# Performance work log

Measured on AMD Instinct MI355X. Metric: run time of the kernel, lower is better.

The kernel has to match this reference:

```python
import jax, jax.numpy as jnp
import numpy as np

H = 1024
NH = 16
HD = H // NH
EPS = 1e-5

def setup_inputs() -> dict:
    key = jax.random.key(0)
    ks = jax.random.split(key, 5)
    B, S = 2, 2048
    scale = 1.0 / np.sqrt(H)
    return {
        "x": jax.random.normal(ks[0], (B, S, H), dtype=jnp.float32),
        "Wq": jax.random.normal(ks[1], (H, H), dtype=jnp.float32) * scale,
        "Wk": jax.random.normal(ks[2], (H, H), dtype=jnp.float32) * scale,
        "Wv": jax.random.normal(ks[3], (H, H), dtype=jnp.float32) * scale,
        "Wo": jax.random.normal(ks[4], (H, H), dtype=jnp.float32) * scale,
        "bo": jnp.zeros((H,), dtype=jnp.float32),
        "gamma": jnp.ones((H,), dtype=jnp.float32),
        "beta": jnp.zeros((H,), dtype=jnp.float32),
    }

def reference(x, Wq, Wk, Wv, Wo, bo, gamma, beta):
    B, S, _ = x.shape
    residual = x
    # pre-LayerNorm
    mu = jnp.mean(x, axis=-1, keepdims=True)
    var = jnp.mean(jnp.square(x - mu), axis=-1, keepdims=True)
    xn = (x - mu) * jax.lax.rsqrt(var + EPS) * gamma + beta
    # QKV projections (torch Linear: y = x @ W.T), split heads -> [B, NH, S, HD]
    q = (xn @ Wq.T).reshape(B, S, NH, HD).transpose(0, 2, 1, 3)
    k = (xn @ Wk.T).reshape(B, S, NH, HD).transpose(0, 2, 1, 3)
    v = (xn @ Wv.T).reshape(B, S, NH, HD).transpose(0, 2, 1, 3)
    # naive attention: explicit [B, NH, S, S] scores
    scale = 1.0 / np.sqrt(HD)
    scores = jnp.einsum('bhqd,bhkd->bhqk', q, k) * scale
    attn = jax.nn.softmax(scores.astype(jnp.float32), axis=-1).astype(q.dtype)
    out = jnp.einsum('bhqk,bhkd->bhqd', attn, v)
    out = out.transpose(0, 2, 1, 3).reshape(B, S, H)
    out = out @ Wo.T + bo
    return out + residual
```

## Files before the change

kernel.cpp:

```cpp
#include <hip/hip_runtime.h>
#include <hip/hip_bf16.h>

#define H 1024
#define NHEAD 16
#define HDIM 64
#define SEQ 2048
#define BATCH 2
#define M_TOT (BATCH * SEQ)
#define NQKV 3072

typedef __attribute__((ext_vector_type(8))) short bf16x8;
typedef __attribute__((ext_vector_type(4))) float f32x4;
typedef __attribute__((ext_vector_type(16))) float f32x16;

#define C2_SCALE 0.18033688f

__device__ __forceinline__ unsigned short f2bf(float f) {
  union { float f; unsigned int u; } a;
  a.f = f;
  unsigned int u = a.u;
  return (unsigned short)((u + 0x7fffu + ((u >> 16) & 1u)) >> 16);
}

__device__ __forceinline__ unsigned int pkbf(float a, float b) {
  union { __hip_bfloat162 h; unsigned int u; } cv;
  cv.h = __float22bfloat162_rn(float2{a, b});
  return cv.u;
}

__device__ __forceinline__ float fast_exp2(float x) {
#if defined(__has_builtin) && __has_builtin(__builtin_amdgcn_exp2f)
  return __builtin_amdgcn_exp2f(x);
#else
  return exp2f(x);
#endif
}

typedef const __attribute__((address_space(1))) void* gas1_t;
typedef __attribute__((address_space(3))) void* las3_t;
__device__ __forceinline__ void gload16(const void* g, void* l) {
  __builtin_amdgcn_global_load_lds((gas1_t)(unsigned long long)g,
                                   (las3_t)(unsigned int)(unsigned long long)l,
                                   16, 0, 0);
}

__global__ __launch_bounds__(256) void ln_cast_kernel(const float* __restrict__ x,
                                                      const float* __restrict__ gamma,
                                                      const float* __restrict__ beta,
                                                      unsigned short* __restrict__ xn,
                                                      const float* __restrict__ w0,
                                                      const float* __restrict__ w1,
                                                      const float* __restrict__ w2,
                                                      const float* __restrict__ w3,
                                                      unsigned short* __restrict__ wdst) {
  const int t = threadIdx.x;
  if (blockIdx.x >= M_TOT) {
    const int cb = blockIdx.x - M_TOT;
    const int y = cb >> 10;
    const float* s = (y == 0) ? w0 : (y == 1) ? w1 : (y == 2) ? w2 : w3;
    const int i = (cb & 1023) * 256 + t;
    const float4 v = ((const float4*)s)[i];
    ushort4 o;
    o.x = f2bf(v.x);
    o.y = f2bf(v.y);
    o.z = f2bf(v.z);
    o.w = f2bf(v.w);
    ((ushort4*)(wdst + (size_t)y * H * H))[i] = o;
    return;
  }
  const int row = blockIdx.x;
  const float* xr = x + (size_t)row * H;
  float4 v = ((const float4*)xr)[t];
  float s = v.x + v.y + v.z + v.w;
  float s2 = v.x * v.x + v.y * v.y + v.z * v.z + v.w * v.w;
#pragma unroll
  for (int o = 32; o; o >>= 1) {
    s += __shfl_xor(s, o, 64);
    s2 += __shfl_xor(s2, o, 64);
  }
  __shared__ float red[8];
  const int wave = t >> 6;
  if ((t & 63) == 0) {
    red[wave] = s;
    red[wave + 4] = s2;
  }
  __syncthreads();
  const float ts = red[0] + red[1] + red[2] + red[3];
  const float ts2 = red[4] + red[5] + red[6] + red[7];
  const float mu = ts * (1.0f / (float)H);
  const float var = ts2 * (1.0f / (float)H) - mu * mu;
  const float rstd = rsqrtf(var + 1e-5f);
  const float4 g = ((const float4*)gamma)[t];
  const float4 b = ((const float4*)beta)[t];
  ushort4 o;
  o.x = f2bf((v.x - mu) * rstd * g.x + b.x);
  o.y = f2bf((v.y - mu) * rstd * g.y + b.y);
  o.z = f2bf((v.z - mu) * rstd * g.z + b.z);
  o.w = f2bf((v.w - mu) * rstd * g.w + b.w);
  ((ushort4*)(xn + (size_t)row * H))[t] = o;
}

template <int EPI, int NPX>
__global__ __launch_bounds__(256, 4) void gemm128(const unsigned short* __restrict__ A,
                                                  const unsigned short* __restrict__ W,
                                                  unsigned short* __restrict__ qk,
                                                  unsigned short* __restrict__ vt,
                                                  const float* __restrict__ bo,
                                                  const float* __restrict__ x,
                                                  float* __restrict__ out) {
  const int id = blockIdx.x;
  const int xcd = id & 7;
  const int r = id >> 3;
  const int nb = xcd * NPX + (r % NPX);
  const int mb = r / NPX;
  const int m0 = mb * 128;
  const int n0 = nb * 128;
  const int tid = threadIdx.x;
  const int wave = tid >> 6;
  const int lane = tid & 63;
  const int l16 = lane & 15;
  const int quad = lane >> 4;
  const int wx = wave & 1, wy = wave >> 1;

  __shared__ __align__(16) unsigned short As[2][128 * 32];
  __shared__ __align__(16) unsigned short Bs[2][128 * 32];

  const int sub = lane >> 2;
  const int kcol = (lane & 3) * 8;
  const unsigned short* ag = A + (size_t)(m0 + wave * 32 + sub) * H + kcol;
  const unsigned short* bg = W + (size_t)(n0 + wave * 32 + sub) * H + kcol;
  const int lofs = wave * 32 * 32;

  f32x4 acc[4][4] = {};

  gload16(ag, &As[0][lofs]);
  gload16(ag + 16 * H, &As[0][lofs + 16 * 32]);
  gload16(bg, &Bs[0][lofs]);
  gload16(bg + 16 * H, &Bs[0][lofs + 16 * 32]);

  for (int it = 0; it < H / 32; it++) {
    const int bi = it & 1;
    __syncthreads();
    if (it + 1 < H / 32) {
      const int k1 = (it + 1) * 32;
      gload16(ag + k1, &As[bi ^ 1][lofs]);
      gload16(ag + k1 + 16 * H, &As[bi ^ 1][lofs + 16 * 32]);
      gload16(bg + k1, &Bs[bi ^ 1][lofs]);
      gload16(bg + k1 + 16 * H, &Bs[bi ^ 1][lofs + 16 * 32]);
    }
    bf16x8 af[4], bf[4];
#pragma unroll
    for (int t = 0; t < 4; t++) {
      af[t] = *(const bf16x8*)&As[bi][(wy * 64 + t * 16 + l16) * 32 + quad * 8];
      bf[t] = *(const bf16x8*)&Bs[bi][(wx * 64 + t * 16 + l16) * 32 + quad * 8];
    }
#pragma unroll
    for (int i = 0; i < 4; i++)
#pragma unroll
      for (int j = 0; j < 4; j++)
        acc[i][j] = __builtin_amdgcn_mfma_f32_16x16x32_bf16(af[i], bf[j], acc[i][j], 0, 0, 0);
  }

  if (EPI == 0) {
#pragma unroll
    for (int j = 0; j < 4; j++) {
      const int cb = n0 + wx * 64 + j * 16;
      if (cb < 2048) {
        const float qs = (cb < 1024) ? C2_SCALE : 1.0f;
#pragma unroll
        for (int i = 0; i < 4; i++) {
          const int row = m0 + wy * 64 + i * 16 + quad * 4;
#pragma unroll
          for (int r2 = 0; r2 < 4; r2++)
            qk[(size_t)(row + r2) * 2048 + cb + l16] = f2bf(acc[i][j][r2] * qs);
        }
      } else {
        const int n = cb + l16 - 2048;
#pragma unroll
        for (int i = 0; i < 4; i++) {
          const int row0 = m0 + wy * 64 + i * 16 + quad * 4;
          const int b = row0 >> 11;
          const int s = row0 & 2047;
          ushort4 p;
          p.x = f2bf(acc[i][j][0]);
          p.y = f2bf(acc[i][j][1]);
          p.z = f2bf(acc[i][j][2]);
          p.w = f2bf(acc[i][j][3]);
          *(ushort4*)&vt[((size_t)b * 1024 + n) * SEQ + s] = p;
        }
      }
    }
  } else {
#pragma unroll
    for (int j = 0; j < 4; j++) {
      const int col = n0 + wx * 64 + j * 16 + l16;
      const float bv = bo[col];
#pragma unroll
      for (int i = 0; i < 4; i++) {
        const int row = m0 + wy * 64 + i * 16 + quad * 4;
#pragma unroll
        for (int r2 = 0; r2 < 4; r2++) {
          const size_t idx = (size_t)(row + r2) * H + col;
          out[idx] = acc[i][j][r2] + bv + x[idx];
        }
      }
    }
  }
}

__global__ __launch_bounds__(256, 2) void attn_kernel(const unsigned short* __restrict__ qk,
                                                      const unsigned short* __restrict__ vt,
                                                      unsigned short* __restrict__ O) {
  const int id = blockIdx.x;
  const int xcd = id & 7;
  const int slot = id >> 3;
  const int qt = slot & 15;
  const int g = slot >> 4;
  const int combo = xcd * 4 + g;
  const int h = combo & 15;
  const int b = combo >> 4;
  const int tid = threadIdx.x;
  const int wave = tid >> 6;
  const int lane = tid & 63;
  const int l31 = lane & 31;
  const int l7 = lane & 7;
  const int hi = lane >> 5;

  __shared__ __align__(16) unsigned short Kt[2][64 * 64];
  __shared__ __align__(16) unsigned short Vt[2][64 * 64];

  const unsigned short* Qbase = qk + (size_t)b * SEQ * 2048 + h * 64;
  const unsigned short* Kbase = qk + (size_t)b * SEQ * 2048 + 1024 + h * 64;
  const unsigned short* Vbase = vt + ((size_t)b * 1024 + h * 64) * SEQ;

  const int rIn = lane >> 3;
  const int gsw = (lane & 7) ^ rIn;
  const int ch0 = 2 * wave;

  const int qrow = qt * 128 + wave * 32 + l31;
  bf16x8 aq[4];
#pragma unroll
  for (int kc = 0; kc < 4; kc++)
    aq[kc] = *(const bf16x8*)(Qbase + (size_t)qrow * 2048 + kc * 16 + hi * 8);

  f32x16 o_acc[2] = {};
  float lc[4] = {};

#pragma unroll
  for (int c = 0; c < 2; c++) {
    const int ch = ch0 + c;
    const int row = ch * 8 + rIn;
    gload16(Kbase + (size_t)row * 2048 + gsw * 8, &Kt[0][ch * 512]);
    gload16(Vbase + (size_t)row * SEQ + gsw * 8, &Vt[0][ch * 512]);
  }

#pragma unroll 2
  for (int it = 0; it < SEQ / 64; it++) {
    const int bi = it & 1;
    __syncthreads();
    if (it + 1 < SEQ / 64) {
#pragma unroll
      for (int c = 0; c < 2; c++) {
        const int ch = ch0 + c;
        const int row = ch * 8 + rIn;
        gload16(Kbase + (size_t)((it + 1) * 64 + row) * 2048 + gsw * 8,
                &Kt[bi ^ 1][ch * 512]);
        gload16(Vbase + (size_t)row * SEQ + (it + 1) * 64 + gsw * 8,
                &Vt[bi ^ 1][ch * 512]);
      }
    }

    f32x16 s_acc[2] = {};
#pragma unroll
    for (int kc = 0; kc < 4; kc++) {
#pragma unroll
      for (int mt = 0; mt < 2; mt++) {
        const bf16x8 kf = *(const bf16x8*)&Kt[bi][(mt * 32 + l31) * 64 +
                                                 ((kc * 16 + hi * 8) ^ (l7 * 8))];
        s_acc[mt] = __builtin_amdgcn_mfma_f32_32x32x16_bf16(kf, aq[kc], s_acc[mt], 0, 0, 0);
      }
    }

    unsigned int w[2][8];
#pragma unroll
    for (int mt = 0; mt < 2; mt++) {
      float p[16];
#pragma unroll
      for (int r2 = 0; r2 < 16; r2++) p[r2] = fast_exp2(s_acc[mt][r2]);
      const float a0 = (p[0] + p[1]) + (p[2] + p[3]);
      const float a1 = (p[4] + p[5]) + (p[6] + p[7]);
      const float a2 = (p[8] + p[9]) + (p[10] + p[11]);
      const float a3 = (p[12] + p[13]) + (p[14] + p[15]);
      lc[mt * 2 + 0] += a0 + a2;
      lc[mt * 2 + 1] += a1 + a3;
#pragma unroll
      for (int gi = 0; gi < 8; gi++) w[mt][gi] = pkbf(p[2 * gi], p[2 * gi + 1]);
    }

#pragma unroll
    for (int sc = 0; sc < 4; sc++) {
      const int n0i = 2 * sc, n1i = 2 * sc + 1;
      const int mt0 = n0i >> 2, b0 = n0i & 3;
      const int mt1 = n1i >> 2, b1 = n1i & 3;
      const auto rA = __builtin_amdgcn_permlane32_swap(w[mt0][2 * b0], w[mt1][2 * b1],
                                                       false, false);
      const auto rB = __builtin_amdgcn_permlane32_swap(w[mt0][2 * b0 + 1], w[mt1][2 * b1 + 1],
                                                       false, false);
      union { unsigned int u[4]; bf16x8 v; } pb;
      pb.u[0] = rA[0];
      pb.u[1] = rB[0];
      pb.u[2] = rA[1];
      pb.u[3] = rB[1];
#pragma unroll
      for (int dt = 0; dt < 2; dt++) {
        const bf16x8 vf = *(const bf16x8*)&Vt[bi][(dt * 32 + l31) * 64 +
                                                  ((sc * 16 + hi * 8) ^ (l7 * 8))];
        o_acc[dt] = __builtin_amdgcn_mfma_f32_32x32x16_bf16(vf, pb.v, o_acc[dt], 0, 0, 0);
      }
    }
  }

  float lsum = (lc[0] + lc[1]) + (lc[2] + lc[3]);
  const float l_i = lsum + __shfl_xor(lsum, 32, 64);
  const float inv = 1.0f / l_i;
  unsigned short* orow = O + ((size_t)(b * SEQ + qrow)) * H + h * 64;
#pragma unroll
  for (int dt = 0; dt < 2; dt++)
#pragma unroll
    for (int rg = 0; rg < 4; rg++) {
      uint2 d;
      d.x = pkbf(o_acc[dt][4 * rg + 0] * inv, o_acc[dt][4 * rg + 1] * inv);
      d.y = pkbf(o_acc[dt][4 * rg + 2] * inv, o_acc[dt][4 * rg + 3] * inv);
      *(uint2*)&orow[dt * 32 + 8 * rg + 4 * hi] = d;
    }
}

extern "C" void kernel_launch(void* const* d_in, const int* in_sizes, int n_in,
                              void* d_out, int out_size, void* d_ws, size_t ws_size,
                              hipStream_t stream) {
  const float* x = (const float*)d_in[0];
  const float* Wq = (const float*)d_in[1];
  const float* Wk = (const float*)d_in[2];
  const float* Wv = (const float*)d_in[3];
  const float* Wo = (const float*)d_in[4];
  const float* bo = (const float*)d_in[5];
  const float* gamma = (const float*)d_in[6];
  const float* beta = (const float*)d_in[7];
  float* out = (float*)d_out;

  unsigned short* ws = (unsigned short*)d_ws;
  unsigned short* xn = ws;
  unsigned short* wcat = xn + (size_t)M_TOT * H;
  unsigned short* wob = wcat + (size_t)3 * H * H;
  unsigned short* qkb = wcat + (size_t)4 * H * H;
  unsigned short* vtb = qkb + (size_t)M_TOT * 2048;
  unsigned short* atb = vtb + (size_t)BATCH * H * SEQ;

  ln_cast_kernel<<<M_TOT + 4096, 256, 0, stream>>>(x, gamma, beta, xn, Wq, Wk, Wv, Wo,
                                                   wcat);
  gemm128<0, 3><<<(M_TOT / 128) * (NQKV / 128), 256, 0, stream>>>(
      xn, wcat, qkb, vtb, nullptr, nullptr, nullptr);
  attn_kernel<<<(SEQ / 128) * NHEAD * BATCH, 256, 0, stream>>>(qkb, vtb, atb);
  gemm128<1, 1><<<(M_TOT / 128) * (H / 128), 256, 0, stream>>>(
      atb, wob, nullptr, nullptr, bo, x, out);
}
```

Before: 191.3 us.

## Split attention key tiles across wave pairs and shrink query tile to 64

The attention kernel now handles 64 query rows per block instead of 128. Each pair of waves splits every 64-key tile in half, so each wave computes one 32x32 score block instead of two. Partial O accumulators and row sums from waves 2-3 are reduced through shared memory, reusing the K buffer, before the normalized write. Grid size doubles and launch bounds go up to 4 blocks per CU to improve occupancy and parallelism, at the cost of loading each K/V tile twice as often per query row and adding a final reduction step.

```diff
diff --git a/kernel.cpp b/kernel.cpp
--- a/kernel.cpp
+++ b/kernel.cpp
@@ -208,14 +208,14 @@
   }
 }
 
-__global__ __launch_bounds__(256, 2) void attn_kernel(const unsigned short* __restrict__ qk,
+__global__ __launch_bounds__(256, 4) void attn_kernel(const unsigned short* __restrict__ qk,
                                                       const unsigned short* __restrict__ vt,
                                                       unsigned short* __restrict__ O) {
   const int id = blockIdx.x;
   const int xcd = id & 7;
   const int slot = id >> 3;
-  const int qt = slot & 15;
-  const int g = slot >> 4;
+  const int qt = slot & 31;
+  const int g = slot >> 5;
   const int combo = xcd * 4 + g;
   const int h = combo & 15;
   const int b = combo >> 4;
@@ -225,9 +225,12 @@
   const int l31 = lane & 31;
   const int l7 = lane & 7;
   const int hi = lane >> 5;
+  const int strip = wave & 1;
+  const int sh = wave >> 1;
 
   __shared__ __align__(16) unsigned short Kt[2][64 * 64];
   __shared__ __align__(16) unsigned short Vt[2][64 * 64];
+  __shared__ float lred[128];
 
   const unsigned short* Qbase = qk + (size_t)b * SEQ * 2048 + h * 64;
   const unsigned short* Kbase = qk + (size_t)b * SEQ * 2048 + 1024 + h * 64;
@@ -237,14 +240,14 @@
   const int gsw = (lane & 7) ^ rIn;
   const int ch0 = 2 * wave;
 
-  const int qrow = qt * 128 + wave * 32 + l31;
+  const int qrow = qt * 64 + strip * 32 + l31;
   bf16x8 aq[4];
 #pragma unroll
   for (int kc = 0; kc < 4; kc++)
     aq[kc] = *(const bf16x8*)(Qbase + (size_t)qrow * 2048 + kc * 16 + hi * 8);
 
   f32x16 o_acc[2] = {};
-  float lc[4] = {};
+  float lc[2] = {};
 
 #pragma unroll
   for (int c = 0; c < 2; c++) {
@@ -270,47 +273,41 @@
       }
     }
 
-    f32x16 s_acc[2] = {};
+    f32x16 s_acc = {};
 #pragma unroll
     for (int kc = 0; kc < 4; kc++) {
-#pragma unroll
-      for (int mt = 0; mt < 2; mt++) {
-        const bf16x8 kf = *(const bf16x8*)&Kt[bi][(mt * 32 + l31) * 64 +
-                                                 ((kc * 16 + hi * 8) ^ (l7 * 8))];
-        s_acc[mt] = __builtin_amdgcn_mfma_f32_32x32x16_bf16(kf, aq[kc], s_acc[mt], 0, 0, 0);
-      }
-    }
-
-    unsigned int w[2][8];
-#pragma unroll
-    for (int mt = 0; mt < 2; mt++) {
-      float p[16];
-#pragma unroll
-      for (int r2 = 0; r2 < 16; r2++) p[r2] = fast_exp2(s_acc[mt][r2]);
+      const bf16x8 kf = *(const bf16x8*)&Kt[bi][(sh * 32 + l31) * 64 +
+                                               ((kc * 16 + hi * 8) ^ (l7 * 8))];
+      s_acc = __builtin_amdgcn_mfma_f32_32x32x16_bf16(kf, aq[kc], s_acc, 0, 0, 0);
+    }
+
+    float p[16];
+#pragma unroll
+    for (int r2 = 0; r2 < 16; r2++) p[r2] = fast_exp2(s_acc[r2]);
+    {
       const float a0 = (p[0] + p[1]) + (p[2] + p[3]);
       const float a1 = (p[4] + p[5]) + (p[6] + p[7]);
       const float a2 = (p[8] + p[9]) + (p[10] + p[11]);
       const float a3 = (p[12] + p[13]) + (p[14] + p[15]);
-      lc[mt * 2 + 0] += a0 + a2;
-      lc[mt * 2 + 1] += a1 + a3;
-#pragma unroll
-      for (int gi = 0; gi < 8; gi++) w[mt][gi] = pkbf(p[2 * gi], p[2 * gi + 1]);
-    }
-
-#pragma unroll
-    for (int sc = 0; sc < 4; sc++) {
-      const int n0i = 2 * sc, n1i = 2 * sc + 1;
-      const int mt0 = n0i >> 2, b0 = n0i & 3;
-      const int mt1 = n1i >> 2, b1 = n1i & 3;
-      const auto rA = __builtin_amdgcn_permlane32_swap(w[mt0][2 * b0], w[mt1][2 * b1],
+      lc[0] += a0 + a2;
+      lc[1] += a1 + a3;
+    }
+    unsigned int w[8];
+#pragma unroll
+    for (int gi = 0; gi < 8; gi++) w[gi] = pkbf(p[2 * gi], p[2 * gi + 1]);
+
+#pragma unroll
+    for (int scp = 0; scp < 2; scp++) {
+      const auto rA = __builtin_amdgcn_permlane32_swap(w[4 * scp + 0], w[4 * scp + 2],
                                                        false, false);
-      const auto rB = __builtin_amdgcn_permlane32_swap(w[mt0][2 * b0 + 1], w[mt1][2 * b1 + 1],
+      const auto rB = __builtin_amdgcn_permlane32_swap(w[4 * scp + 1], w[4 * scp + 3],
                                                        false, false);
       union { unsigned int u[4]; bf16x8 v; } pb;
       pb.u[0] = rA[0];
       pb.u[1] = rB[0];
       pb.u[2] = rA[1];
       pb.u[3] = rB[1];
+      const int sc = sh * 2 + scp;
 #pragma unroll
       for (int dt = 0; dt < 2; dt++) {
         const bf16x8 vf = *(const bf16x8*)&Vt[bi][(dt * 32 + l31) * 64 +
@@ -320,19 +317,46 @@
     }
   }
 
-  float lsum = (lc[0] + lc[1]) + (lc[2] + lc[3]);
-  const float l_i = lsum + __shfl_xor(lsum, 32, 64);
-  const float inv = 1.0f / l_i;
-  unsigned short* orow = O + ((size_t)(b * SEQ + qrow)) * H + h * 64;
-#pragma unroll
-  for (int dt = 0; dt < 2; dt++)
-#pragma unroll
-    for (int rg = 0; rg < 4; rg++) {
-      uint2 d;
-      d.x = pkbf(o_acc[dt][4 * rg + 0] * inv, o_acc[dt][4 * rg + 1] * inv);
-      d.y = pkbf(o_acc[dt][4 * rg + 2] * inv, o_acc[dt][4 * rg + 3] * inv);
-      *(uint2*)&orow[dt * 32 + 8 * rg + 4 * hi] = d;
-    }
+  float lsum = lc[0] + lc[1];
+  __syncthreads();
+  if (wave >= 2) {
+    float4* obuf4 = (float4*)&Kt[0][0] + (size_t)(wave - 2) * 512;
+#pragma unroll
+    for (int dt = 0; dt < 2; dt++)
+#pragma unroll
+      for (int rg = 0; rg < 4; rg++)
+        obuf4[(dt * 4 + rg) * 64 + lane] =
+            float4{o_acc[dt][4 * rg + 0], o_acc[dt][4 * rg + 1],
+                   o_acc[dt][4 * rg + 2], o_acc[dt][4 * rg + 3]};
+    lred[(wave - 2) * 64 + lane] = lsum;
+  }
+  __syncthreads();
+  if (wave < 2) {
+    const float4* obuf4 = (const float4*)&Kt[0][0] + (size_t)wave * 512;
+#pragma unroll
+    for (int dt = 0; dt < 2; dt++)
+#pragma unroll
+      for (int rg = 0; rg < 4; rg++) {
+        const float4 pv4 = obuf4[(dt * 4 + rg) * 64 + lane];
+        o_acc[dt][4 * rg + 0] += pv4.x;
+        o_acc[dt][4 * rg + 1] += pv4.y;
+        o_acc[dt][4 * rg + 2] += pv4.z;
+        o_acc[dt][4 * rg + 3] += pv4.w;
+      }
+    lsum += lred[wave * 64 + lane];
+    const float l_i = lsum + __shfl_xor(lsum, 32, 64);
+    const float inv = 1.0f / l_i;
+    unsigned short* orow = O + ((size_t)(b * SEQ + qrow)) * H + h * 64;
+#pragma unroll
+    for (int dt = 0; dt < 2; dt++)
+#pragma unroll
+      for (int rg = 0; rg < 4; rg++) {
+        uint2 d;
+        d.x = pkbf(o_acc[dt][4 * rg + 0] * inv, o_acc[dt][4 * rg + 1] * inv);
+        d.y = pkbf(o_acc[dt][4 * rg + 2] * inv, o_acc[dt][4 * rg + 3] * inv);
+        *(uint2*)&orow[dt * 32 + 8 * rg + 4 * hi] = d;
+      }
+  }
 }
 
 extern "C" void kernel_launch(void* const* d_in, const int* in_sizes, int n_in,
@@ -360,7 +384,7 @@
                                                    wcat);
   gemm128<0, 3><<<(M_TOT / 128) * (NQKV / 128), 256, 0, stream>>>(
       xn, wcat, qkb, vtb, nullptr, nullptr, nullptr);
-  attn_kernel<<<(SEQ / 128) * NHEAD * BATCH, 256, 0, stream>>>(qkb, vtb, atb);
+  attn_kernel<<<(SEQ / 64) * NHEAD * BATCH, 256, 0, stream>>>(qkb, vtb, atb);
   gemm128<1, 1><<<(M_TOT / 128) * (H / 128), 256, 0, stream>>>(
       atb, wob, nullptr, nullptr, bo, x, out);
 }
```

Result: no change. 195.0 us (+1.9%).

## Load K/V fragments directly from global into registers, dropping LDS staging

Applied to the files above, without the earlier changes.

The attention kernel no longer stages K and V tiles in shared memory behind a barrier. Each wave loads its MFMA operand fragments for K and V straight from global memory into registers and prefetches the next tile's fragments while the current tile computes. This removes the LDS traffic and the per-iteration __syncthreads. In exchange, each of the four waves now fetches the same K/V data separately, which raises global/L2 traffic fourfold, and the prefetch buffers add register pressure.

```diff
diff --git a/kernel.cpp b/kernel.cpp
--- a/kernel.cpp
+++ b/kernel.cpp
@@ -223,78 +223,77 @@
   const int wave = tid >> 6;
   const int lane = tid & 63;
   const int l31 = lane & 31;
-  const int l7 = lane & 7;
   const int hi = lane >> 5;
-
-  __shared__ __align__(16) unsigned short Kt[2][64 * 64];
-  __shared__ __align__(16) unsigned short Vt[2][64 * 64];
 
   const unsigned short* Qbase = qk + (size_t)b * SEQ * 2048 + h * 64;
   const unsigned short* Kbase = qk + (size_t)b * SEQ * 2048 + 1024 + h * 64;
   const unsigned short* Vbase = vt + ((size_t)b * 1024 + h * 64) * SEQ;
 
-  const int rIn = lane >> 3;
-  const int gsw = (lane & 7) ^ rIn;
-  const int ch0 = 2 * wave;
-
   const int qrow = qt * 128 + wave * 32 + l31;
   bf16x8 aq[4];
 #pragma unroll
   for (int kc = 0; kc < 4; kc++)
     aq[kc] = *(const bf16x8*)(Qbase + (size_t)qrow * 2048 + kc * 16 + hi * 8);
 
+  const unsigned short* kp0 = Kbase + (size_t)l31 * 2048 + hi * 8;
+  const unsigned short* kp1 = Kbase + (size_t)(32 + l31) * 2048 + hi * 8;
+  const unsigned short* vp0 = Vbase + (size_t)l31 * SEQ + hi * 8;
+  const unsigned short* vp1 = Vbase + (size_t)(32 + l31) * SEQ + hi * 8;
+
   f32x16 o_acc[2] = {};
   float lc[4] = {};
 
-#pragma unroll
-  for (int c = 0; c < 2; c++) {
-    const int ch = ch0 + c;
-    const int row = ch * 8 + rIn;
-    gload16(Kbase + (size_t)row * 2048 + gsw * 8, &Kt[0][ch * 512]);
-    gload16(Vbase + (size_t)row * SEQ + gsw * 8, &Vt[0][ch * 512]);
+  bf16x8 kf[2][4];
+  bf16x8 vf[4][2];
+#pragma unroll
+  for (int kc = 0; kc < 4; kc++) {
+    kf[0][kc] = *(const bf16x8*)(kp0 + kc * 16);
+    kf[1][kc] = *(const bf16x8*)(kp1 + kc * 16);
+  }
+#pragma unroll
+  for (int sc = 0; sc < 4; sc++) {
+    vf[sc][0] = *(const bf16x8*)(vp0 + sc * 16);
+    vf[sc][1] = *(const bf16x8*)(vp1 + sc * 16);
   }
 
 #pragma unroll 2
   for (int it = 0; it < SEQ / 64; it++) {
-    const int bi = it & 1;
-    __syncthreads();
-    if (it + 1 < SEQ / 64) {
-#pragma unroll
-      for (int c = 0; c < 2; c++) {
-        const int ch = ch0 + c;
-        const int row = ch * 8 + rIn;
-        gload16(Kbase + (size_t)((it + 1) * 64 + row) * 2048 + gsw * 8,
-                &Kt[bi ^ 1][ch * 512]);
-        gload16(Vbase + (size_t)row * SEQ + (it + 1) * 64 + gsw * 8,
-                &Vt[bi ^ 1][ch * 512]);
+    const int itn = (it + 1 < SEQ / 64) ? it + 1 : (SEQ / 64 - 1);
+
+    f32x16 s0 = {}, s1 = {};
+#pragma unroll
+    for (int kc = 0; kc < 4; kc++) {
+      s0 = __builtin_amdgcn_mfma_f32_32x32x16_bf16(kf[0][kc], aq[kc], s0, 0, 0, 0);
+      s1 = __builtin_amdgcn_mfma_f32_32x32x16_bf16(kf[1][kc], aq[kc], s1, 0, 0, 0);
+    }
+
+    {
+      const size_t ko = (size_t)itn * (64 * 2048);
+#pragma unroll
+      for (int kc = 0; kc < 4; kc++) {
+        kf[0][kc] = *(const bf16x8*)(kp0 + ko + kc * 16);
+        kf[1][kc] = *(const bf16x8*)(kp1 + ko + kc * 16);
       }
     }
 
-    f32x16 s_acc[2] = {};
-#pragma unroll
-    for (int kc = 0; kc < 4; kc++) {
-#pragma unroll
-      for (int mt = 0; mt < 2; mt++) {
-        const bf16x8 kf = *(const bf16x8*)&Kt[bi][(mt * 32 + l31) * 64 +
-                                                 ((kc * 16 + hi * 8) ^ (l7 * 8))];
-        s_acc[mt] = __builtin_amdgcn_mfma_f32_32x32x16_bf16(kf, aq[kc], s_acc[mt], 0, 0, 0);
-      }
-    }
-
     unsigned int w[2][8];
-#pragma unroll
-    for (int mt = 0; mt < 2; mt++) {
+    {
       float p[16];
 #pragma unroll
-      for (int r2 = 0; r2 < 16; r2++) p[r2] = fast_exp2(s_acc[mt][r2]);
-      const float a0 = (p[0] + p[1]) + (p[2] + p[3]);
-      const float a1 = (p[4] + p[5]) + (p[6] + p[7]);
-      const float a2 = (p[8] + p[9]) + (p[10] + p[11]);
-      const float a3 = (p[12] + p[13]) + (p[14] + p[15]);
-      lc[mt * 2 + 0] += a0 + a2;
-      lc[mt * 2 + 1] += a1 + a3;
-#pragma unroll
-      for (int gi = 0; gi < 8; gi++) w[mt][gi] = pkbf(p[2 * gi], p[2 * gi + 1]);
+      for (int r2 = 0; r2 < 16; r2++) p[r2] = fast_exp2(s0[r2]);
+      lc[0] += ((p[0] + p[1]) + (p[2] + p[3])) + ((p[8] + p[9]) + (p[10] + p[11]));
+      lc[1] += ((p[4] + p[5]) + (p[6] + p[7])) + ((p[12] + p[13]) + (p[14] + p[15]));
+#pragma unroll
+      for (int gi = 0; gi < 8; gi++) w[0][gi] = pkbf(p[2 * gi], p[2 * gi + 1]);
+    }
+    {
+      float p[16];
+#pragma unroll
+      for (int r2 = 0; r2 < 16; r2++) p[r2] = fast_exp2(s1[r2]);
+      lc[2] += ((p[0] + p[1]) + (p[2] + p[3])) + ((p[8] + p[9]) + (p[10] + p[11]));
+      lc[3] += ((p[4] + p[5]) + (p[6] + p[7])) + ((p[12] + p[13]) + (p[14] + p[15]));
+#pragma unroll
+      for (int gi = 0; gi < 8; gi++) w[1][gi] = pkbf(p[2 * gi], p[2 * gi + 1]);
     }
 
 #pragma unroll
@@ -311,11 +310,16 @@
       pb.u[1] = rB[0];
       pb.u[2] = rA[1];
       pb.u[3] = rB[1];
-#pragma unroll
-      for (int dt = 0; dt < 2; dt++) {
-        const bf16x8 vf = *(const bf16x8*)&Vt[bi][(dt * 32 + l31) * 64 +
-                                                  ((sc * 16 + hi * 8) ^ (l7 * 8))];
-        o_acc[dt] = __builtin_amdgcn_mfma_f32_32x32x16_bf16(vf, pb.v, o_acc[dt], 0, 0, 0);
+      o_acc[0] = __builtin_amdgcn_mfma_f32_32x32x16_bf16(vf[sc][0], pb.v, o_acc[0], 0, 0, 0);
+      o_acc[1] = __builtin_amdgcn_mfma_f32_32x32x16_bf16(vf[sc][1], pb.v, o_acc[1], 0, 0, 0);
+    }
+
+    {
+      const size_t vo = (size_t)itn * 64;
+#pragma unroll
+      for (int sc = 0; sc < 4; sc++) {
+        vf[sc][0] = *(const bf16x8*)(vp0 + vo + sc * 16);
+        vf[sc][1] = *(const bf16x8*)(vp1 + vo + sc * 16);
       }
     }
   }
```

Result: slower. 266.0 us (+39.0%).

## Software-pipeline attention loop so PV MFMAs overlap next tile's softmax

Applied to the files above, without the earlier changes.

Restructures the attention main loop into a prologue, a steady state and an epilogue. Each iteration issues the QK^T MFMAs for tile i and the PV MFMAs for tile i-1, using exp'd probabilities and V fragments kept in registers from the previous iteration. The exp/pack work then runs after the matrix ops so it can overlap with them. s_setprio is raised around the MFMA blocks to favour matrix issue across waves. The cost is higher register pressure from holding wP and the vfP V fragments across iterations, which could lower occupancy or cause spills.

```diff
diff --git a/kernel.cpp b/kernel.cpp
--- a/kernel.cpp
+++ b/kernel.cpp
@@ -246,6 +246,9 @@
   f32x16 o_acc[2] = {};
   float lc[4] = {};
 
+  unsigned int wP[2][8];
+  bf16x8 vfP[4][2];
+
 #pragma unroll
   for (int c = 0; c < 2; c++) {
     const int ch = ch0 + c;
@@ -254,8 +257,51 @@
     gload16(Vbase + (size_t)row * SEQ + gsw * 8, &Vt[0][ch * 512]);
   }
 
-#pragma unroll 2
-  for (int it = 0; it < SEQ / 64; it++) {
+  {
+    __syncthreads();
+#pragma unroll
+    for (int c = 0; c < 2; c++) {
+      const int ch = ch0 + c;
+      const int row = ch * 8 + rIn;
+      gload16(Kbase + (size_t)(64 + row) * 2048 + gsw * 8, &Kt[1][ch * 512]);
+      gload16(Vbase + (size_t)row * SEQ + 64 + gsw * 8, &Vt[1][ch * 512]);
+    }
+    f32x16 s0 = {}, s1 = {};
+    __builtin_amdgcn_s_setprio(1);
+#pragma unroll
+    for (int kc = 0; kc < 4; kc++) {
+      const bf16x8 kf0 = *(const bf16x8*)&Kt[0][(l31)*64 + ((kc * 16 + hi * 8) ^ (l7 * 8))];
+      const bf16x8 kf1 = *(const bf16x8*)&Kt[0][(32 + l31) * 64 + ((kc * 16 + hi * 8) ^ (l7 * 8))];
+      s0 = __builtin_amdgcn_mfma_f32_32x32x16_bf16(kf0, aq[kc], s0, 0, 0, 0);
+      s1 = __builtin_amdgcn_mfma_f32_32x32x16_bf16(kf1, aq[kc], s1, 0, 0, 0);
+    }
+    __builtin_amdgcn_s_setprio(0);
+    {
+      float p[16];
+#pragma unroll
+      for (int r2 = 0; r2 < 16; r2++) p[r2] = fast_exp2(s0[r2]);
+      lc[0] += ((p[0] + p[1]) + (p[2] + p[3])) + ((p[8] + p[9]) + (p[10] + p[11]));
+      lc[1] += ((p[4] + p[5]) + (p[6] + p[7])) + ((p[12] + p[13]) + (p[14] + p[15]));
+#pragma unroll
+      for (int gi = 0; gi < 8; gi++) wP[0][gi] = pkbf(p[2 * gi], p[2 * gi + 1]);
+    }
+    {
+      float p[16];
+#pragma unroll
+      for (int r2 = 0; r2 < 16; r2++) p[r2] = fast_exp2(s1[r2]);
+      lc[2] += ((p[0] + p[1]) + (p[2] + p[3])) + ((p[8] + p[9]) + (p[10] + p[11]));
+      lc[3] += ((p[4] + p[5]) + (p[6] + p[7])) + ((p[12] + p[13]) + (p[14] + p[15]));
+#pragma unroll
+      for (int gi = 0; gi < 8; gi++) wP[1][gi] = pkbf(p[2 * gi], p[2 * gi + 1]);
+    }
+#pragma unroll
+    for (int sc = 0; sc < 4; sc++) {
+      vfP[sc][0] = *(const bf16x8*)&Vt[0][(l31)*64 + ((sc * 16 + hi * 8) ^ (l7 * 8))];
+      vfP[sc][1] = *(const bf16x8*)&Vt[0][(32 + l31) * 64 + ((sc * 16 + hi * 8) ^ (l7 * 8))];
+    }
+  }
+
+  for (int it = 1; it < SEQ / 64; it++) {
     const int bi = it & 1;
     __syncthreads();
     if (it + 1 < SEQ / 64) {
@@ -270,31 +316,14 @@
       }
     }
 
-    f32x16 s_acc[2] = {};
+    f32x16 s0 = {}, s1 = {};
+    __builtin_amdgcn_s_setprio(1);
 #pragma unroll
     for (int kc = 0; kc < 4; kc++) {
-#pragma unroll
-      for (int mt = 0; mt < 2; mt++) {
-        const bf16x8 kf = *(const bf16x8*)&Kt[bi][(mt * 32 + l31) * 64 +
-                                                 ((kc * 16 + hi * 8) ^ (l7 * 8))];
-        s_acc[mt] = __builtin_amdgcn_mfma_f32_32x32x16_bf16(kf, aq[kc], s_acc[mt], 0, 0, 0);
-      }
-    }
-
-    unsigned int w[2][8];
-#pragma unroll
-    for (int mt = 0; mt < 2; mt++) {
-      float p[16];
-#pragma unroll
-      for (int r2 = 0; r2 < 16; r2++) p[r2] = fast_exp2(s_acc[mt][r2]);
-      const float a0 = (p[0] + p[1]) + (p[2] + p[3]);
-      const float a1 = (p[4] + p[5]) + (p[6] + p[7]);
-      const float a2 = (p[8] + p[9]) + (p[10] + p[11]);
-      const float a3 = (p[12] + p[13]) + (p[14] + p[15]);
-      lc[mt * 2 + 0] += a0 + a2;
-      lc[mt * 2 + 1] += a1 + a3;
-#pragma unroll
-      for (int gi = 0; gi < 8; gi++) w[mt][gi] = pkbf(p[2 * gi], p[2 * gi + 1]);
+      const bf16x8 kf0 = *(const bf16x8*)&Kt[bi][(l31)*64 + ((kc * 16 + hi * 8) ^ (l7 * 8))];
+      const bf16x8 kf1 = *(const bf16x8*)&Kt[bi][(32 + l31) * 64 + ((kc * 16 + hi * 8) ^ (l7 * 8))];
+      s0 = __builtin_amdgcn_mfma_f32_32x32x16_bf16(kf0, aq[kc], s0, 0, 0, 0);
+      s1 = __builtin_amdgcn_mfma_f32_32x32x16_bf16(kf1, aq[kc], s1, 0, 0, 0);
     }
 
 #pragma unroll
@@ -302,23 +331,65 @@
       const int n0i = 2 * sc, n1i = 2 * sc + 1;
       const int mt0 = n0i >> 2, b0 = n0i & 3;
       const int mt1 = n1i >> 2, b1 = n1i & 3;
-      const auto rA = __builtin_amdgcn_permlane32_swap(w[mt0][2 * b0], w[mt1][2 * b1],
+      const auto rA = __builtin_amdgcn_permlane32_swap(wP[mt0][2 * b0], wP[mt1][2 * b1],
                                                        false, false);
-      const auto rB = __builtin_amdgcn_permlane32_swap(w[mt0][2 * b0 + 1], w[mt1][2 * b1 + 1],
+      const auto rB = __builtin_amdgcn_permlane32_swap(wP[mt0][2 * b0 + 1], wP[mt1][2 * b1 + 1],
                                                        false, false);
       union { unsigned int u[4]; bf16x8 v; } pb;
       pb.u[0] = rA[0];
       pb.u[1] = rB[0];
       pb.u[2] = rA[1];
       pb.u[3] = rB[1];
-#pragma unroll
-      for (int dt = 0; dt < 2; dt++) {
-        const bf16x8 vf = *(const bf16x8*)&Vt[bi][(dt * 32 + l31) * 64 +
-                                                  ((sc * 16 + hi * 8) ^ (l7 * 8))];
-        o_acc[dt] = __builtin_amdgcn_mfma_f32_32x32x16_bf16(vf, pb.v, o_acc[dt], 0, 0, 0);
-      }
-    }
-  }
+      o_acc[0] = __builtin_amdgcn_mfma_f32_32x32x16_bf16(vfP[sc][0], pb.v, o_acc[0], 0, 0, 0);
+      o_acc[1] = __builtin_amdgcn_mfma_f32_32x32x16_bf16(vfP[sc][1], pb.v, o_acc[1], 0, 0, 0);
+    }
+    __builtin_amdgcn_s_setprio(0);
+
+    {
+      float p[16];
+#pragma unroll
+      for (int r2 = 0; r2 < 16; r2++) p[r2] = fast_exp2(s0[r2]);
+      lc[0] += ((p[0] + p[1]) + (p[2] + p[3])) + ((p[8] + p[9]) + (p[10] + p[11]));
+      lc[1] += ((p[4] + p[5]) + (p[6] + p[7])) + ((p[12] + p[13]) + (p[14] + p[15]));
+#pragma unroll
+      for (int gi = 0; gi < 8; gi++) wP[0][gi] = pkbf(p[2 * gi], p[2 * gi + 1]);
+    }
+    {
+      float p[16];
+#pragma unroll
+      for (int r2 = 0; r2 < 16; r2++) p[r2] = fast_exp2(s1[r2]);
+      lc[2] += ((p[0] + p[1]) + (p[2] + p[3])) + ((p[8] + p[9]) + (p[10] + p[11]));
+      lc[3] += ((p[4] + p[5]) + (p[6] + p[7])) + ((p[12] + p[13]) + (p[14] + p[15]));
+#pragma unroll
+      for (int gi = 0; gi < 8; gi++) wP[1][gi] = pkbf(p[2 * gi], p[2 * gi + 1]);
+    }
+
+#pragma unroll
+    for (int sc = 0; sc < 4; sc++) {
+      vfP[sc][0] = *(const bf16x8*)&Vt[bi][(l31)*64 + ((sc * 16 + hi * 8) ^ (l7 * 8))];
+      vfP[sc][1] = *(const bf16x8*)&Vt[bi][(32 + l31) * 64 + ((sc * 16 + hi * 8) ^ (l7 * 8))];
+    }
+  }
+
+  __builtin_amdgcn_s_setprio(1);
+#pragma unroll
+  for (int sc = 0; sc < 4; sc++) {
+    const int n0i = 2 * sc, n1i = 2 * sc + 1;
+    const int mt0 = n0i >> 2, b0 = n0i & 3;
+    const int mt1 = n1i >> 2, b1 = n1i & 3;
+    const auto rA = __builtin_amdgcn_permlane32_swap(wP[mt0][2 * b0], wP[mt1][2 * b1],
+                                                     false, false);
+    const auto rB = __builtin_amdgcn_permlane32_swap(wP[mt0][2 * b0 + 1], wP[mt1][2 * b1 + 1],
+                                                     false, false);
+    union { unsigned int u[4]; bf16x8 v; } pb;
+    pb.u[0] = rA[0];
+    pb.u[1] = rB[0];
+    pb.u[2] = rA[1];
+    pb.u[3] = rB[1];
+    o_acc[0] = __builtin_amdgcn_mfma_f32_32x32x16_bf16(vfP[sc][0], pb.v, o_acc[0], 0, 0, 0);
+    o_acc[1] = __builtin_amdgcn_mfma_f32_32x32x16_bf16(vfP[sc][1], pb.v, o_acc[1], 0, 0, 0);
+  }
+  __builtin_amdgcn_s_setprio(0);
 
   float lsum = (lc[0] + lc[1]) + (lc[2] + lc[3]);
   const float l_i = lsum + __shfl_xor(lsum, 32, 64);
```

Result: no change. 194.2 us (+1.5%).
